# Kernel optimization log

Hardware: AMD Instinct MI355X
Metric: run time of the kernel (lower is better)

Reference implementation:

```python
import jax, jax.numpy as jnp
import numpy as np

NEG_SLOPE = 0.2
MASK_FILL = -1e9


def setup_inputs() -> dict:
    key = jax.random.key(0)
    k1, k2, k3, k4 = jax.random.split(key, 4)
    B, N, IN_DIM = 4, 2048, 256
    H, D = 8, 64  # n_heads, hidden_dim (out_dim)
    nodes = jax.random.normal(k1, (B, N, IN_DIM), dtype=jnp.float32)
    edges = jax.random.randint(k2, (B, N, N), 0, 2, dtype=jnp.int32)
    # Xavier-uniform-ish init for params
    pw_lim = float(np.sqrt(6.0 / (IN_DIM + H * D)))
    proj_weights = jax.random.uniform(k3, (IN_DIM, H * D), dtype=jnp.float32,
                                      minval=-pw_lim, maxval=pw_lim)
    aw_lim = float(np.sqrt(6.0 / (H + 2 * D)))
    attn_weights = jax.random.uniform(k4, (H, 2 * D), dtype=jnp.float32,
                                      minval=-aw_lim, maxval=aw_lim)
    return {"nodes": nodes, "edges": edges,
            "proj_weights": proj_weights, "attn_weights": attn_weights}


def reference(nodes, edges, proj_weights, attn_weights):
    B, N, _ = nodes.shape
    H, twoD = attn_weights.shape
    D = twoD // 2
    # Projection: [B,N,in] @ [in,H*D] -> [B,H,N,D]
    mapped = jnp.matmul(nodes, proj_weights).reshape(B, N, H, D).transpose(0, 2, 1, 3)
    # The left@diag(a)@right^T trick is exactly a_l.h_i + a_r.h_j:
    a_l = attn_weights[:, :D]   # [H,D]
    a_r = attn_weights[:, D:]   # [H,D]
    el = jnp.einsum('bhnd,hd->bhn', mapped, a_l)  # score contribution of source i
    er = jnp.einsum('bhnd,hd->bhn', mapped, a_r)  # score contribution of target j
    scores = jax.nn.leaky_relu(el[:, :, :, None] + er[:, :, None, :],
                               negative_slope=NEG_SLOPE)  # [B,H,N,N]
    scores = jnp.where(edges[:, None, :, :] == 0, MASK_FILL, scores)
    attn = jax.nn.softmax(scores, axis=-1)  # dropout p=0 -> identity
    out = jnp.einsum('bhij,bhjd->bhid', attn, mapped)  # [B,H,N,D]
    out = out.transpose(0, 2, 1, 3).reshape(B, N, H * D)  # is_concat=True
    return jax.nn.sigmoid(out)
```

## Files before the change

kernel.cpp:

```cpp
#include <hip/hip_runtime.h>
#include <hip/hip_fp16.h>
#include <math.h>

#define NEG 0.2f
#define LOG2E 1.4426950408889634f

typedef float f32x4 __attribute__((ext_vector_type(4)));
typedef _Float16 half8 __attribute__((ext_vector_type(8)));

#if __has_builtin(__builtin_amdgcn_exp2f)
#define EXP2F(x) __builtin_amdgcn_exp2f(x)
#else
#define EXP2F(x) exp2f(x)
#endif

__device__ inline uint cvt2(float a, float b) {
  union {
    decltype(__builtin_amdgcn_cvt_pkrtz(0.f, 0.f)) v;
    uint u;
  } x;
  x.v = __builtin_amdgcn_cvt_pkrtz(a, b);
  return x.u;
}

__global__ __launch_bounds__(256) void prep_kernel(const float* __restrict__ W,
                                                   ushort* __restrict__ wf,
                                                   uint* __restrict__ ermx) {
  const int bx = blockIdx.x;
  const int t = threadIdx.x;
  if (bx == 32) {
    if (t < 32) ermx[t] = 0u;
    return;
  }
  const int h = bx >> 2, ct = bx & 3;
#pragma unroll
  for (int s = 0; s < 2; ++s) {
    int slot = t + s * 256;
    int l = slot & 63, kk = slot >> 6;
    int col = h * 64 + ct * 16 + (l & 15);
    int k0 = kk * 32 + (l >> 4) * 8;
    uint outv[4];
#pragma unroll
    for (int c = 0; c < 4; ++c) {
      float x0 = W[(size_t)(k0 + 2 * c) * 512 + col];
      float x1 = W[(size_t)(k0 + 2 * c + 1) * 512 + col];
      outv[c] = cvt2(x0, x1);
    }
    *(uint4*)&wf[(((size_t)((h * 4 + ct) * 8 + kk)) * 64 + l) * 8] = *(uint4*)outv;
  }
}

__global__ __launch_bounds__(256) void pack_edges(const int* __restrict__ e,
                                                  unsigned long long* __restrict__ epk64) {
  const int wid = blockIdx.x * 4 + (threadIdx.x >> 6);
  const int l = threadIdx.x & 63;
  const size_t base = (size_t)wid * 1024;
#pragma unroll
  for (int it = 0; it < 4; ++it) {
    const size_t off = base + it * 256;
    unsigned long long b0 = __ballot(e[off + l] != 0);
    unsigned long long b1 = __ballot(e[off + 64 + l] != 0);
    unsigned long long b2 = __ballot(e[off + 128 + l] != 0);
    unsigned long long b3 = __ballot(e[off + 192 + l] != 0);
    if (l == 0) {
      ulonglong2 p0, p1;
      p0.x = b0;
      p0.y = b1;
      p1.x = b2;
      p1.y = b3;
      *(ulonglong2*)&epk64[off >> 6] = p0;
      *(ulonglong2*)&epk64[(off >> 6) + 2] = p1;
    }
  }
}

__global__ __launch_bounds__(256, 4) void proj_mfma(
    const float* __restrict__ A, const ushort* __restrict__ wf,
    const float* __restrict__ aw, ushort* __restrict__ mt,
    float* __restrict__ el, float* __restrict__ er, uint* __restrict__ ermx) {
  __shared__ ushort ct_lds[64][72];
  const int t = threadIdx.x;
  const int wq = t >> 6, l = t & 63;
  const int i0 = blockIdx.x * 64;
  const int h = blockIdx.y;
  const int b = i0 >> 11, n0 = i0 & 2047, bh = b * 8 + h;
  const int cl = l & 15, hi = l >> 4;
  const float* arow = A + (size_t)(i0 + wq * 16 + cl) * 256 + hi * 8;
  const int4* wfb = (const int4*)wf + (size_t)h * 32 * 64 + l;
  f32x4 acc[4];
#pragma unroll
  for (int ct = 0; ct < 4; ++ct) acc[ct] = (f32x4){0.f, 0.f, 0.f, 0.f};
#pragma unroll
  for (int kk = 0; kk < 8; ++kk) {
    float4 a0 = *(const float4*)(arow + kk * 32);
    float4 a1 = *(const float4*)(arow + kk * 32 + 4);
    union {
      uint u[4];
      half8 v;
    } af;
    af.u[0] = cvt2(a0.x, a0.y);
    af.u[1] = cvt2(a0.z, a0.w);
    af.u[2] = cvt2(a1.x, a1.y);
    af.u[3] = cvt2(a1.z, a1.w);
#pragma unroll
    for (int ct = 0; ct < 4; ++ct) {
      union {
        int4 i;
        half8 v;
      } bf;
      bf.i = wfb[((size_t)ct * 8 + kk) * 64];
      acc[ct] = __builtin_amdgcn_mfma_f32_16x16x32_f16(af.v, bf.v, acc[ct], 0, 0, 0);
    }
  }
  float alc[4], arc[4];
#pragma unroll
  for (int ct = 0; ct < 4; ++ct) {
    alc[ct] = aw[h * 128 + ct * 16 + cl];
    arc[ct] = aw[h * 128 + 64 + ct * 16 + cl];
  }
  float ermax_loc = -1e30f;
#pragma unroll
  for (int reg = 0; reg < 4; ++reg) {
    float pl = acc[0][reg] * alc[0] + acc[1][reg] * alc[1] + acc[2][reg] * alc[2] +
               acc[3][reg] * alc[3];
    float pr = acc[0][reg] * arc[0] + acc[1][reg] * arc[1] + acc[2][reg] * arc[2] +
               acc[3][reg] * arc[3];
#pragma unroll
    for (int s = 1; s < 16; s <<= 1) {
      pl += __shfl_xor(pl, s);
      pr += __shfl_xor(pr, s);
    }
    if (cl == 0) {
      int n = n0 + wq * 16 + hi * 4 + reg;
      el[(size_t)bh * 2048 + n] = pl;
      er[(size_t)bh * 2048 + n] = pr;
    }
    ermax_loc = fmaxf(ermax_loc, pr);
  }
  ermax_loc = fmaxf(ermax_loc, __shfl_xor(ermax_loc, 16));
  ermax_loc = fmaxf(ermax_loc, __shfl_xor(ermax_loc, 32));
  if (l == 0) {
    uint bits = __float_as_uint(ermax_loc);
    uint key = (bits & 0x80000000u) ? ~bits : (bits | 0x80000000u);
    atomicMax(&ermx[bh], key);
  }
#pragma unroll
  for (int ct = 0; ct < 4; ++ct) {
    ushort4 us;
    us.x = __half_as_ushort(__float2half(acc[ct][0]));
    us.y = __half_as_ushort(__float2half(acc[ct][1]));
    us.z = __half_as_ushort(__float2half(acc[ct][2]));
    us.w = __half_as_ushort(__float2half(acc[ct][3]));
    *(ushort4*)&ct_lds[ct * 16 + cl][wq * 16 + hi * 4] = us;
  }
  __syncthreads();
  {
    const int f = t >> 5, s = t & 31;
    const int g = f >> 2, nt = f & 3;
    const int r = nt * 16 + (s & 15);
    const int cm = g * 32 + (s >> 4) * 8;
    int4 v0 = *(const int4*)&ct_lds[r][cm];
    int4 v1 = *(const int4*)&ct_lds[r][cm + 16];
    const size_t base = ((size_t)bh * 32 + (n0 >> 6)) * 4096 + f * 512;
    *(int4*)&mt[base + s * 8] = v0;
    *(int4*)&mt[base + (s + 32) * 8] = v1;
  }
}

__global__ __launch_bounds__(512, 8) void gat_attn(const ushort* __restrict__ mt,
                                                   const uint* __restrict__ epk,
                                                   const float* __restrict__ el,
                                                   const float* __restrict__ er,
                                                   const uint* __restrict__ ermx,
                                                   float* __restrict__ out) {
  __shared__ __align__(16) char smem[40960];
  int4* vt4 = (int4*)smem;
  float* er_s = (float*)(smem + 32768);
  const int t = threadIdx.x;
  const int l = t & 63;
  const int hf = t >> 8;
  const int th = t & 255;
  const int wq = (t >> 6) & 3;
  const int r16 = l & 15, hi = l >> 4;
  const int sh8 = hi * 8;
  const int i0 = blockIdx.x * 64;
  const int h = blockIdx.y, b = blockIdx.z;
  const int bh = b * 8 + h;
  *(float4*)&er_s[t * 4] = *(const float4*)&er[(size_t)bh * 2048 + t * 4];
  const int irow = i0 + wq * 16 + r16;
  const float el_r = el[(size_t)bh * 2048 + irow];
  const uint ky = ermx[bh];
  const float emx = __uint_as_float((ky & 0x80000000u) ? (ky ^ 0x80000000u) : ~ky);
  const float s0 = el_r + emx;
  const float m_r = fmaxf(s0, NEG * s0);
  const float m2 = m_r * LOG2E;
  const float cA = __builtin_fmaf(el_r, LOG2E, -m2);
  const float cB = __builtin_fmaf(el_r, NEG * LOG2E, -m2);
  const uint* erow = epk + (size_t)(b * 2048 + irow) * 64;
  f32x4 acc[4];
  f32x4 accL = {0.f, 0.f, 0.f, 0.f};
#pragma unroll
  for (int nt = 0; nt < 4; ++nt) acc[nt] = (f32x4){0.f, 0.f, 0.f, 0.f};
  half8 ones;
#pragma unroll
  for (int c = 0; c < 8; ++c) ones[c] = (_Float16)1.f;

  const int jtg0 = hf * 16;
  const int4* srcbase = (const int4*)mt + ((size_t)bh * 32 + jtg0) * 512 + wq * 128 + l;
  unsigned long long ew = *(const unsigned long long*)(erow + jtg0 * 2);
  {
    int4 p0 = srcbase[0];
    int4 p1 = srcbase[64];
    int4* d = vt4 + hf * 512 + wq * 128 + l;
    d[0] = p0;
    d[64] = p1;
  }
  __syncthreads();
  int cur = 0;
  for (int jt = 0; jt < 16; ++jt) {
    int4 nx0, nx1;
    unsigned long long ewn;
    if (jt < 15) {
      const int4* s = srcbase + (size_t)(jt + 1) * 512;
      nx0 = s[0];
      nx1 = s[64];
      ewn = *(const unsigned long long*)(erow + (jtg0 + jt + 1) * 2);
    }
    const uint wsh0 = ((uint)ew) >> sh8;
    const uint wsh1 = ((uint)(ew >> 32)) >> sh8;
    const int j0 = (jtg0 + jt) * 64;
    half8 af[2];
#pragma unroll
    for (int g = 0; g < 2; ++g) {
      float4 u0 = *(const float4*)&er_s[j0 + g * 32 + sh8];
      float4 u1 = *(const float4*)&er_s[j0 + g * 32 + sh8 + 4];
      float uv[8] = {u0.x, u0.y, u0.z, u0.w, u1.x, u1.y, u1.z, u1.w};
      const uint wg = g ? wsh1 : wsh0;
      float pv[8];
#pragma unroll
      for (int c = 0; c < 8; ++c) {
        float a = __builtin_fmaf(uv[c], LOG2E, cA);
        float bq = __builtin_fmaf(uv[c], NEG * LOG2E, cB);
        float tt = fmaxf(a, bq);
        float p = EXP2F(tt);
        pv[c] = (wg & (1u << c)) ? p : 0.f;
      }
      union {
        uint u[4];
        half8 v8;
      } fr;
#pragma unroll
      for (int c = 0; c < 4; ++c) fr.u[c] = cvt2(pv[2 * c], pv[2 * c + 1]);
      af[g] = fr.v8;
    }
    const half8* fb = (const half8*)(vt4 + cur * 1024 + hf * 512);
    __builtin_amdgcn_s_setprio(1);
#pragma unroll
    for (int g = 0; g < 2; ++g) {
      accL = __builtin_amdgcn_mfma_f32_16x16x32_f16(af[g], ones, accL, 0, 0, 0);
#pragma unroll
      for (int nt = 0; nt < 4; ++nt) {
        half8 bfr = fb[(g * 4 + nt) * 64 + l];
        acc[nt] = __builtin_amdgcn_mfma_f32_16x16x32_f16(af[g], bfr, acc[nt], 0, 0, 0);
      }
    }
    __builtin_amdgcn_s_setprio(0);
    if (jt < 15) {
      int4* d = vt4 + (cur ^ 1) * 1024 + hf * 512 + wq * 128 + l;
      d[0] = nx0;
      d[64] = nx1;
      ew = ewn;
    }
    __syncthreads();
    cur ^= 1;
  }
  float* red = (float*)smem;
  if (hf == 1) {
    float* dst = red + th * 21;
#pragma unroll
    for (int nt = 0; nt < 4; ++nt)
#pragma unroll
      for (int k = 0; k < 4; ++k) dst[nt * 4 + k] = acc[nt][k];
#pragma unroll
    for (int k = 0; k < 4; ++k) dst[16 + k] = accL[k];
  }
  __syncthreads();
  if (hf == 0) {
    const float* src = red + th * 21;
#pragma unroll
    for (int reg = 0; reg < 4; ++reg) {
      float Lrow = accL[reg] + src[16 + reg];
      float invL = 1.f / Lrow;
      int orow = i0 + wq * 16 + hi * 4 + reg;
#pragma unroll
      for (int nt = 0; nt < 4; ++nt) {
        float o = (acc[nt][reg] + src[nt * 4 + reg]) * invL;
        float sig = 1.f / (1.f + __expf(-o));
        out[(size_t)(b * 2048 + orow) * 512 + h * 64 + nt * 16 + r16] = sig;
      }
    }
  }
}

extern "C" void kernel_launch(void* const* d_in, const int* in_sizes, int n_in,
                              void* d_out, int out_size, void* d_ws, size_t ws_size,
                              hipStream_t stream) {
  const float* nodes = (const float*)d_in[0];
  const int* edges = (const int*)d_in[1];
  const float* pw = (const float*)d_in[2];
  const float* aw = (const float*)d_in[3];
  float* out = (float*)d_out;

  ushort* mt = (ushort*)d_ws;
  float* el = (float*)((char*)d_ws + 8388608);
  float* er = (float*)((char*)d_ws + 8650752);
  uint* ermx = (uint*)((char*)d_ws + 8912896);
  uint* epk = (uint*)((char*)d_ws + 8913024);
  ushort* wf = (ushort*)((char*)d_ws + 11010176);

  prep_kernel<<<33, 256, 0, stream>>>(pw, (ushort*)wf, ermx);
  pack_edges<<<4096, 256, 0, stream>>>(edges, (unsigned long long*)epk);
  proj_mfma<<<dim3(128, 8), 256, 0, stream>>>(nodes, wf, aw, mt, el, er, ermx);
  gat_attn<<<dim3(32, 8, 4), 512, 0, stream>>>(mt, epk, el, er, ermx, out);
}
```

Before: 104.9 us.

## Fuse edge packing into projection kernel and compute softmax scores in packed fp16

The edge bit-packing and projection kernels become a single launch in which blocks are interleaved, four pack blocks per projection block, so the two memory-bound and compute-bound phases run concurrently and one launch is dropped. In the attention kernel, er is stored in LDS as fp16, and the leaky-relu score and exponent are computed with packed half2 FMA/max plus an fp16 exp2, with the edge mask applied as a bitwise AND. This halves the LDS footprint for er and aims to cut VALU work in the hot loop. The cost is precision: score arguments carry fp16 rounding error before exponentiation, which could perturb the attention weights.

```diff
diff --git a/kernel.cpp b/kernel.cpp
--- a/kernel.cpp
+++ b/kernel.cpp
@@ -7,12 +7,9 @@
 
 typedef float f32x4 __attribute__((ext_vector_type(4)));
 typedef _Float16 half8 __attribute__((ext_vector_type(8)));
-
-#if __has_builtin(__builtin_amdgcn_exp2f)
-#define EXP2F(x) __builtin_amdgcn_exp2f(x)
-#else
-#define EXP2F(x) exp2f(x)
-#endif
+typedef _Float16 h2v __attribute__((ext_vector_type(2)));
+
+extern "C" __device__ _Float16 __ocml_exp2_f16(_Float16);
 
 __device__ inline uint cvt2(float a, float b) {
   union {
@@ -20,6 +17,24 @@
     uint u;
   } x;
   x.v = __builtin_amdgcn_cvt_pkrtz(a, b);
+  return x.u;
+}
+
+__device__ inline h2v u2h(uint u) {
+  union {
+    uint u;
+    h2v v;
+  } x;
+  x.u = u;
+  return x.v;
+}
+
+__device__ inline uint h2u(h2v v) {
+  union {
+    uint u;
+    h2v v;
+  } x;
+  x.v = v;
   return x.u;
 }
 
@@ -50,39 +65,42 @@
   }
 }
 
-__global__ __launch_bounds__(256) void pack_edges(const int* __restrict__ e,
-                                                  unsigned long long* __restrict__ epk64) {
-  const int wid = blockIdx.x * 4 + (threadIdx.x >> 6);
-  const int l = threadIdx.x & 63;
-  const size_t base = (size_t)wid * 1024;
-#pragma unroll
-  for (int it = 0; it < 4; ++it) {
-    const size_t off = base + it * 256;
-    unsigned long long b0 = __ballot(e[off + l] != 0);
-    unsigned long long b1 = __ballot(e[off + 64 + l] != 0);
-    unsigned long long b2 = __ballot(e[off + 128 + l] != 0);
-    unsigned long long b3 = __ballot(e[off + 192 + l] != 0);
-    if (l == 0) {
-      ulonglong2 p0, p1;
-      p0.x = b0;
-      p0.y = b1;
-      p1.x = b2;
-      p1.y = b3;
-      *(ulonglong2*)&epk64[off >> 6] = p0;
-      *(ulonglong2*)&epk64[(off >> 6) + 2] = p1;
-    }
-  }
-}
-
-__global__ __launch_bounds__(256, 4) void proj_mfma(
+__global__ __launch_bounds__(256, 4) void pack_proj(
+    const int* __restrict__ e, unsigned long long* __restrict__ epk64,
     const float* __restrict__ A, const ushort* __restrict__ wf,
     const float* __restrict__ aw, ushort* __restrict__ mt,
     float* __restrict__ el, float* __restrict__ er, uint* __restrict__ ermx) {
   __shared__ ushort ct_lds[64][72];
+  const int bx = blockIdx.x;
   const int t = threadIdx.x;
-  const int wq = t >> 6, l = t & 63;
-  const int i0 = blockIdx.x * 64;
-  const int h = blockIdx.y;
+  const int l = t & 63;
+  if (bx % 5 != 4) {
+    const int pack_id = (bx / 5) * 4 + (bx % 5);
+    const int wid = pack_id * 4 + (t >> 6);
+    const size_t base = (size_t)wid * 1024;
+#pragma unroll
+    for (int it = 0; it < 4; ++it) {
+      const size_t off = base + it * 256;
+      unsigned long long b0 = __ballot(e[off + l] != 0);
+      unsigned long long b1 = __ballot(e[off + 64 + l] != 0);
+      unsigned long long b2 = __ballot(e[off + 128 + l] != 0);
+      unsigned long long b3 = __ballot(e[off + 192 + l] != 0);
+      if (l == 0) {
+        ulonglong2 p0, p1;
+        p0.x = b0;
+        p0.y = b1;
+        p1.x = b2;
+        p1.y = b3;
+        *(ulonglong2*)&epk64[off >> 6] = p0;
+        *(ulonglong2*)&epk64[(off >> 6) + 2] = p1;
+      }
+    }
+    return;
+  }
+  const int pid = bx / 5;
+  const int wq = t >> 6;
+  const int i0 = (pid & 127) * 64;
+  const int h = pid >> 7;
   const int b = i0 >> 11, n0 = i0 & 2047, bh = b * 8 + h;
   const int cl = l & 15, hi = l >> 4;
   const float* arow = A + (size_t)(i0 + wq * 16 + cl) * 256 + hi * 8;
@@ -173,9 +191,9 @@
                                                    const float* __restrict__ er,
                                                    const uint* __restrict__ ermx,
                                                    float* __restrict__ out) {
-  __shared__ __align__(16) char smem[40960];
+  __shared__ __align__(16) char smem[36864];
   int4* vt4 = (int4*)smem;
-  float* er_s = (float*)(smem + 32768);
+  uint* ersh = (uint*)(smem + 32768);
   const int t = threadIdx.x;
   const int l = t & 63;
   const int hf = t >> 8;
@@ -186,7 +204,16 @@
   const int i0 = blockIdx.x * 64;
   const int h = blockIdx.y, b = blockIdx.z;
   const int bh = b * 8 + h;
-  *(float4*)&er_s[t * 4] = *(const float4*)&er[(size_t)bh * 2048 + t * 4];
+  if (t < 256) {
+    float4 e0 = *(const float4*)&er[(size_t)bh * 2048 + t * 8];
+    float4 e1 = *(const float4*)&er[(size_t)bh * 2048 + t * 8 + 4];
+    uint4 pk;
+    pk.x = cvt2(e0.x, e0.y);
+    pk.y = cvt2(e0.z, e0.w);
+    pk.z = cvt2(e1.x, e1.y);
+    pk.w = cvt2(e1.z, e1.w);
+    *(uint4*)&ersh[t * 4] = pk;
+  }
   const int irow = i0 + wq * 16 + r16;
   const float el_r = el[(size_t)bh * 2048 + irow];
   const uint ky = ermx[bh];
@@ -194,8 +221,12 @@
   const float s0 = el_r + emx;
   const float m_r = fmaxf(s0, NEG * s0);
   const float m2 = m_r * LOG2E;
-  const float cA = __builtin_fmaf(el_r, LOG2E, -m2);
-  const float cB = __builtin_fmaf(el_r, NEG * LOG2E, -m2);
+  const float cAf = __builtin_fmaf(el_r, LOG2E, -m2);
+  const float cBf = __builtin_fmaf(el_r, NEG * LOG2E, -m2);
+  const h2v cA2 = {(_Float16)cAf, (_Float16)cAf};
+  const h2v cB2 = {(_Float16)cBf, (_Float16)cBf};
+  const h2v l2e2 = {(_Float16)LOG2E, (_Float16)LOG2E};
+  const h2v nl2e2 = {(_Float16)(NEG * LOG2E), (_Float16)(NEG * LOG2E)};
   const uint* erow = epk + (size_t)(b * 2048 + irow) * 64;
   f32x4 acc[4];
   f32x4 accL = {0.f, 0.f, 0.f, 0.f};
@@ -232,25 +263,33 @@
     half8 af[2];
 #pragma unroll
     for (int g = 0; g < 2; ++g) {
-      float4 u0 = *(const float4*)&er_s[j0 + g * 32 + sh8];
-      float4 u1 = *(const float4*)&er_s[j0 + g * 32 + sh8 + 4];
-      float uv[8] = {u0.x, u0.y, u0.z, u0.w, u1.x, u1.y, u1.z, u1.w};
+      uint4 uv = *(const uint4*)&ersh[(j0 >> 1) + g * 16 + hi * 4];
+      uint uvw[4] = {uv.x, uv.y, uv.z, uv.w};
       const uint wg = g ? wsh1 : wsh0;
-      float pv[8];
-#pragma unroll
-      for (int c = 0; c < 8; ++c) {
-        float a = __builtin_fmaf(uv[c], LOG2E, cA);
-        float bq = __builtin_fmaf(uv[c], NEG * LOG2E, cB);
-        float tt = fmaxf(a, bq);
-        float p = EXP2F(tt);
-        pv[c] = (wg & (1u << c)) ? p : 0.f;
-      }
       union {
         uint u[4];
         half8 v8;
       } fr;
 #pragma unroll
-      for (int c = 0; c < 4; ++c) fr.u[c] = cvt2(pv[2 * c], pv[2 * c + 1]);
+      for (int q = 0; q < 4; ++q) {
+        h2v u2 = u2h(uvw[q]);
+#if __has_builtin(__builtin_elementwise_fma)
+        h2v a2 = __builtin_elementwise_fma(u2, l2e2, cA2);
+        h2v b2 = __builtin_elementwise_fma(u2, nl2e2, cB2);
+#else
+        h2v a2 = u2 * l2e2 + cA2;
+        h2v b2 = u2 * nl2e2 + cB2;
+#endif
+        h2v t2 = __builtin_elementwise_max(a2, b2);
+        h2v p2;
+        p2[0] = __ocml_exp2_f16(t2[0]);
+        p2[1] = __ocml_exp2_f16(t2[1]);
+        uint pu = h2u(p2);
+        uint mlo = (uint)(((int)(wg << (31 - 2 * q))) >> 31);
+        uint mhi = (uint)(((int)(wg << (30 - 2 * q))) >> 31);
+        uint mask2 = (mlo & 0x0000FFFFu) | (mhi & 0xFFFF0000u);
+        fr.u[q] = pu & mask2;
+      }
       af[g] = fr.v8;
     }
     const half8* fb = (const half8*)(vt4 + cur * 1024 + hf * 512);
@@ -318,8 +357,8 @@
   uint* epk = (uint*)((char*)d_ws + 8913024);
   ushort* wf = (ushort*)((char*)d_ws + 11010176);
 
-  prep_kernel<<<33, 256, 0, stream>>>(pw, (ushort*)wf, ermx);
-  pack_edges<<<4096, 256, 0, stream>>>(edges, (unsigned long long*)epk);
-  proj_mfma<<<dim3(128, 8), 256, 0, stream>>>(nodes, wf, aw, mt, el, er, ermx);
+  prep_kernel<<<33, 256, 0, stream>>>(pw, wf, ermx);
+  pack_proj<<<5120, 256, 0, stream>>>(edges, (unsigned long long*)epk, nodes, wf, aw,
+                                      mt, el, er, ermx);
   gat_attn<<<dim3(32, 8, 4), 512, 0, stream>>>(mt, epk, el, er, ermx, out);
 }
```

Measured after the change: 91.33 us. 12.9% less time.
